# Kernel tuning notes

Measured on AMD Instinct MI355X. Metric: run time of the kernel, lower is better.

The kernel has to match this reference:

```python
import jax, jax.numpy as jnp
import numpy as np

K = 4
EPS = 1e-5
NEG_SLOPE = 0.2


def _edge_feature(coor_q, x_q, coor_k, x_k, k):
    """coor_*: [B,3,G*], x_q: [B,C,Gq], x_k: [B,C,Gk] -> [B,2C,Gq,k]"""
    B = x_k.shape[0]
    cq = jax.lax.stop_gradient(coor_q)
    ck = jax.lax.stop_gradient(coor_k)
    # squared pairwise distances [B, Gq, Gk]
    q2 = jnp.sum(cq * cq, axis=1)  # [B,Gq]
    k2 = jnp.sum(ck * ck, axis=1)  # [B,Gk]
    dist = q2[:, :, None] + k2[:, None, :] - 2.0 * jnp.einsum('bcq,bck->bqk', cq, ck)
    _, idx = jax.lax.top_k(-dist, k)  # k nearest, idx: [B,Gq,k]
    xk_t = jnp.transpose(x_k, (0, 2, 1))  # [B,Gk,C]
    feat = xk_t[jnp.arange(B)[:, None, None], idx]  # [B,Gq,k,C] gather
    feat = jnp.transpose(feat, (0, 3, 1, 2))  # [B,C,Gq,k]
    xq = jnp.broadcast_to(x_q[:, :, :, None], feat.shape)
    return jnp.concatenate([feat - xq, xq], axis=1)


def _group_norm(x, gamma, beta, groups):
    # x: [B,C,G,k], normalize per (group, sample) over (C//groups, G, k)
    B, C, G, k = x.shape
    xr = x.reshape(B, groups, -1)
    mean = jnp.mean(xr, axis=-1, keepdims=True)
    var = jnp.var(xr, axis=-1, keepdims=True)
    xn = ((xr - mean) * jax.lax.rsqrt(var + EPS)).reshape(B, C, G, k)
    return xn * gamma[None, :, None, None] + beta[None, :, None, None]


def _block(x, W, gamma, beta):
    # 1x1 conv (no bias) + GroupNorm(4) + LeakyReLU(0.2)
    y = jnp.einsum('oc,bcgk->bogk', W, x)
    y = _group_norm(y, gamma, beta, 4)
    return jax.nn.leaky_relu(y, NEG_SLOPE)


def setup_inputs() -> dict:
    key = jax.random.key(0)
    ks = jax.random.split(key, 10)
    B, C, Gs, Gd = 16, 384, 4096, 1024
    return {
        'coor': jax.random.normal(ks[0], (B, 3, Gs), jnp.float32),
        'f': jax.random.normal(ks[1], (B, C, Gs), jnp.float32),
        'coor_q': jax.random.normal(ks[2], (B, 3, Gd), jnp.float32),
        'f_q': jax.random.normal(ks[3], (B, C, Gd), jnp.float32),
        'W1': jax.random.normal(ks[4], (512, 2 * C), jnp.float32) * 0.02,
        'g1': jnp.ones((512,), jnp.float32),
        'b1': jnp.zeros((512,), jnp.float32),
        'W2': jax.random.normal(ks[5], (C, 1024), jnp.float32) * 0.02,
        'g2': jnp.ones((C,), jnp.float32),
        'b2': jnp.zeros((C,), jnp.float32),
    }


def reference(coor, f, coor_q, f_q, W1, g1, b1, W2, g2, b2):
    e1 = _edge_feature(coor_q, f_q, coor, f, K)        # [B,768,Gd,k]
    h = jnp.max(_block(e1, W1, g1, b1), axis=-1)       # [B,512,Gd]
    e2 = _edge_feature(coor_q, h, coor_q, h, K)        # [B,1024,Gd,k]
    out = jnp.max(_block(e2, W2, g2, b2), axis=-1)     # [B,384,Gd]
    return out
```

## Files before the change

kernel.cpp:

```cpp
#include <hip/hip_runtime.h>
#include <stdint.h>

#define B_   16
#define CIN  384
#define GS   4096
#define GD   1024
#define M1   512
#define K2C  512
#define M2   384
#define ROWS2 768
#define NEG  0.2f
#define EPS_ 1e-5f

typedef __bf16 bf16x8 __attribute__((ext_vector_type(8)));
typedef float  f32x4  __attribute__((ext_vector_type(4)));
typedef float  f32x2  __attribute__((ext_vector_type(2)));
typedef unsigned long long u64k;

__device__ __forceinline__ float bf2f(ushort u) {
  uint32_t v = ((uint32_t)u) << 16;
  return __builtin_bit_cast(float, v);
}
__device__ __forceinline__ ushort f2bf(float f) {
  uint32_t x = __builtin_bit_cast(uint32_t, f);
  x += 0x7FFFu + ((x >> 16) & 1u);
  return (ushort)(x >> 16);
}

__device__ __forceinline__ f32x2 pk_mul(f32x2 a, f32x2 b) {
  f32x2 d; asm("v_pk_mul_f32 %0, %1, %2" : "=v"(d) : "v"(a), "v"(b)); return d;
}
__device__ __forceinline__ f32x2 pk_add(f32x2 a, f32x2 b) {
  f32x2 d; asm("v_pk_add_f32 %0, %1, %2" : "=v"(d) : "v"(a), "v"(b)); return d;
}
__device__ __forceinline__ f32x2 pk_fma(f32x2 a, f32x2 b, f32x2 c) {
  f32x2 d; asm("v_pk_fma_f32 %0, %1, %2, %3" : "=v"(d) : "v"(a), "v"(b), "v"(c)); return d;
}

__device__ __forceinline__ void gload16(const void* g, void* l) {
  __builtin_amdgcn_global_load_lds(
      (const __attribute__((address_space(1))) void*)g,
      (__attribute__((address_space(3))) void*)l, 16, 0, 0);
}

__global__ void k_transpose(const float* __restrict__ src, ushort* __restrict__ dst,
                            int Cdim, int N) {
  __shared__ ushort tile[32][33];
  int b = blockIdx.z;
  int n0 = blockIdx.x * 32, c0 = blockIdx.y * 32;
  const float* s = src + (size_t)b * Cdim * N;
  ushort* d = dst + (size_t)b * Cdim * N;
  int tx = threadIdx.x, ty = threadIdx.y;
#pragma unroll
  for (int i = 0; i < 4; i++) {
    int c = c0 + ty + i * 8;
    tile[ty + i * 8][tx] = f2bf(s[(size_t)c * N + n0 + tx]);
  }
  __syncthreads();
#pragma unroll
  for (int i = 0; i < 4; i++) {
    int n = n0 + ty + i * 8;
    d[(size_t)n * Cdim + c0 + tx] = tile[tx][ty + i * 8];
  }
}

__global__ void k_wprep2(const float* __restrict__ W1, const float* __restrict__ W2,
                         ushort* __restrict__ W1a, ushort* __restrict__ W1d,
                         ushort* __restrict__ W2a, ushort* __restrict__ W2d) {
  int blk = blockIdx.x;
  if (blk < 768) {
    int t = blk * 256 + threadIdx.x;
    int o = t / 384, c = t % 384;
    float wa = W1[(size_t)o * 768 + c];
    float wb = W1[(size_t)o * 768 + 384 + c];
    W1a[t] = f2bf(wa);
    W1d[t] = f2bf(wb - wa);
  } else {
    int t = (blk - 768) * 256 + threadIdx.x;
    int o = t / 512, c = t % 512;
    float wa = W2[(size_t)o * 1024 + c];
    float wb = W2[(size_t)o * 1024 + 512 + c];
    W2a[t] = f2bf(wa);
    W2d[t] = f2bf(wb - wa);
  }
}

__global__ void k_s2both(const float* __restrict__ cs, const float* __restrict__ cq,
                         float* __restrict__ s2s, float* __restrict__ s2q) {
#pragma clang fp contract(off)
  int b = blockIdx.z;
  int i = blockIdx.x * 256 + threadIdx.x;
  if (i < GS) {
    const float* cb = cs + (size_t)b * 3 * GS;
    float x = cb[i], y = cb[GS + i], z = cb[2 * GS + i];
    s2s[(size_t)b * GS + i] = (x * x + y * y) + z * z;
  } else {
    int j = i - GS;
    const float* cb = cq + (size_t)b * 3 * GD;
    float x = cb[j], y = cb[GD + j], z = cb[2 * GD + j];
    s2q[(size_t)b * GD + j] = (x * x + y * y) + z * z;
  }
}

__device__ __forceinline__ uint32_t dmap(float d) {
  uint32_t u = __builtin_bit_cast(uint32_t, d);
  return u ^ (((uint32_t)((int32_t)u >> 31)) | 0x80000000u);
}
__device__ __forceinline__ u64k mkkey(uint32_t hi, uint32_t lo) {
  uint2 t; t.x = lo; t.y = hi;
  return __builtin_bit_cast(u64k, t);
}
__device__ __forceinline__ void kce(u64k& a, u64k& b) {
  bool c = b < a;
  u64k lo = c ? b : a, hi = c ? a : b;
  a = lo; b = hi;
}
__device__ __forceinline__ void klmin(u64k& a, u64k b) { a = b < a ? b : a; }

template<int GSRC>
__global__ __launch_bounds__(256) void k_knn(const float* __restrict__ cq,
                                             const float* __restrict__ ck,
                                             const float* __restrict__ s2qry,
                                             const float* __restrict__ s2src,
                                             int* __restrict__ idx) {
  constexpr int ITERS = GSRC / 256;
  static_assert(ITERS % 2 == 0, "even iteration count required for 2-deep unroll");
  int tid = threadIdx.x;
  int lane = tid & 63, wv = tid >> 6;
  int b = blockIdx.y;
  int qA = blockIdx.x * 8 + wv * 2;
  int qB = qA + 1;
  const float* cqb = cq + (size_t)b * 3 * GD;
  const float* ckb = ck + (size_t)b * 3 * GSRC;
  const float* s2b = s2src + (size_t)b * GSRC;
  float qxA = cqb[qA], qyA = cqb[GD + qA], qzA = cqb[2 * GD + qA];
  float qxB = cqb[qB], qyB = cqb[GD + qB], qzB = cqb[2 * GD + qB];
  float q2A = s2qry[(size_t)b * GD + qA];
  float q2B = s2qry[(size_t)b * GD + qB];
  f32x2 qxpA = {qxA, qxA}, qypA = {qyA, qyA}, qzpA = {qzA, qzA}, q2pA = {q2A, q2A};
  f32x2 qxpB = {qxB, qxB}, qypB = {qyB, qyB}, qzpB = {qzB, qzB}, q2pB = {q2B, q2B};
  f32x2 m2p = {-2.f, -2.f};

  u64k kA0 = ~0ull, kA1 = ~0ull, kA2 = ~0ull, kA3 = ~0ull;
  u64k kB0 = ~0ull, kB1 = ~0ull, kB2 = ~0ull, kB3 = ~0ull;

#define KNN_Q(QXP, QYP, QZP, Q2P, K0, K1, K2, K3)                              \
  {                                                                            \
    f32x2 dotl = pk_add(pk_add(pk_mul(QXP, xl), pk_mul(QYP, yl)), pk_mul(QZP, zl)); \
    f32x2 doth = pk_add(pk_add(pk_mul(QXP, xh), pk_mul(QYP, yh)), pk_mul(QZP, zh)); \
    f32x2 dl = pk_fma(dotl, m2p, pk_add(Q2P, sl));                             \
    f32x2 dh = pk_fma(doth, m2p, pk_add(Q2P, sh));                             \
    u64k n0 = mkkey(dmap(dl.x), j0u);                                          \
    u64k n1 = mkkey(dmap(dl.y), j0u + 1);                                      \
    u64k n2 = mkkey(dmap(dh.x), j0u + 2);                                      \
    u64k n3 = mkkey(dmap(dh.y), j0u + 3);                                      \
    kce(n0, n1); kce(n2, n3); kce(n0, n2); kce(n1, n3); kce(n1, n2);           \
    klmin(K0, n3); klmin(K1, n2); klmin(K2, n1); klmin(K3, n0);                \
    kce(K0, K2); kce(K1, K3); kce(K0, K1); kce(K2, K3);                        \
  }

#define KNN_STEP(Xv, Yv, Zv, Sv, J0)                                           \
  {                                                                            \
    f32x2 xl = {Xv.x, Xv.y}, xh = {Xv.z, Xv.w};                                \
    f32x2 yl = {Yv.x, Yv.y}, yh = {Yv.z, Yv.w};                                \
    f32x2 zl = {Zv.x, Zv.y}, zh = {Zv.z, Zv.w};                                \
    f32x2 sl = {Sv.x, Sv.y}, sh = {Sv.z, Sv.w};                                \
    uint32_t j0u = (uint32_t)(J0);                                             \
    KNN_Q(qxpA, qypA, qzpA, q2pA, kA0, kA1, kA2, kA3);                         \
    KNN_Q(qxpB, qypB, qzpB, q2pB, kB0, kB1, kB2, kB3);                         \
  }

#define KNN_LOAD(Xv, Yv, Zv, Sv, J)                                            \
  {                                                                            \
    Xv = *reinterpret_cast<const float4*>(ckb + (J));                          \
    Yv = *reinterpret_cast<const float4*>(ckb + GSRC + (J));                   \
    Zv = *reinterpret_cast<const float4*>(ckb + 2 * GSRC + (J));               \
    Sv = *reinterpret_cast<const float4*>(s2b + (J));                          \
  }

  int base = lane * 4;
  float4 X0, Y0, Z0, S0, X1, Y1, Z1, S1;
  KNN_LOAD(X0, Y0, Z0, S0, base);
  for (int it = 0; it < ITERS; it += 2) {
    int j0 = it * 256 + base;
    KNN_LOAD(X1, Y1, Z1, S1, j0 + 256);
    KNN_STEP(X0, Y0, Z0, S0, j0);
    if (it + 2 < ITERS) KNN_LOAD(X0, Y0, Z0, S0, j0 + 512);
    KNN_STEP(X1, Y1, Z1, S1, j0 + 256);
  }
#undef KNN_STEP
#undef KNN_Q
#undef KNN_LOAD

#pragma unroll
  for (int off = 1; off < 64; off <<= 1) {
    u64k p0 = __shfl_xor(kA0, off), p1 = __shfl_xor(kA1, off);
    u64k p2 = __shfl_xor(kA2, off), p3 = __shfl_xor(kA3, off);
    klmin(kA0, p3); klmin(kA1, p2); klmin(kA2, p1); klmin(kA3, p0);
    kce(kA0, kA2); kce(kA1, kA3); kce(kA0, kA1); kce(kA2, kA3);
    u64k r0 = __shfl_xor(kB0, off), r1 = __shfl_xor(kB1, off);
    u64k r2 = __shfl_xor(kB2, off), r3 = __shfl_xor(kB3, off);
    klmin(kB0, r3); klmin(kB1, r2); klmin(kB2, r1); klmin(kB3, r0);
    kce(kB0, kB2); kce(kB1, kB3); kce(kB0, kB1); kce(kB2, kB3);
  }
  if (lane == 0) {
    int4 ra;
    ra.x = (int)(uint32_t)kA0; ra.y = (int)(uint32_t)kA1;
    ra.z = (int)(uint32_t)kA2; ra.w = (int)(uint32_t)kA3;
    *reinterpret_cast<int4*>(&idx[((size_t)b * GD + qA) * 4]) = ra;
    int4 rb;
    rb.x = (int)(uint32_t)kB0; rb.y = (int)(uint32_t)kB1;
    rb.z = (int)(uint32_t)kB2; rb.w = (int)(uint32_t)kB3;
    *reinterpret_cast<int4*>(&idx[((size_t)b * GD + qB) * 4]) = rb;
  }
}

template<bool OUT_BF16>
__global__ __launch_bounds__(256) void k_gemm(const ushort* __restrict__ W,
                                              const ushort* __restrict__ Xt,
                                              void* __restrict__ outv,
                                              int M, int Kd, int N) {
  __shared__ __align__(16) ushort As[128 * 32];
  __shared__ __align__(16) ushort Bs[128 * 32];
  int b = blockIdx.z;
  const ushort* X = Xt + (size_t)b * N * Kd;
  int m0 = blockIdx.y * 128, n0 = blockIdx.x * 128;
  int tid = threadIdx.x;
  int w = tid >> 6, lane = tid & 63;
  int lr = lane & 15, lq = lane >> 4;
  int mw = (w >> 1) * 64, nw = (w & 1) * 64;
  int r0 = tid >> 2, c0 = tid & 3;

  ushort* dA0 = As + w * 512;
  ushort* dA1 = As + 2048 + w * 512;
  ushort* dB0 = Bs + w * 512;
  ushort* dB1 = Bs + 2048 + w * 512;
  const ushort* gA0 = W + (size_t)(m0 + r0) * Kd + c0 * 8;
  const ushort* gA1 = W + (size_t)(m0 + r0 + 64) * Kd + c0 * 8;
  const ushort* gB0 = X + (size_t)(n0 + r0) * Kd + c0 * 8;
  const ushort* gB1 = X + (size_t)(n0 + r0 + 64) * Kd + c0 * 8;

  f32x4 zero = {0.f, 0.f, 0.f, 0.f};
  f32x4 acc[4][4];
#pragma unroll
  for (int mi = 0; mi < 4; mi++)
#pragma unroll
    for (int ni = 0; ni < 4; ni++) acc[mi][ni] = zero;

  int nk = Kd / 32;
  for (int kt = 0; kt < nk; kt++) {
    int kk = kt * 32;
    __syncthreads();
    gload16(gA0 + kk, dA0);
    gload16(gA1 + kk, dA1);
    gload16(gB0 + kk, dB0);
    gload16(gB1 + kk, dB1);
    __syncthreads();
    bf16x8 af[4], bfr[4];
#pragma unroll
    for (int mi = 0; mi < 4; mi++)
      af[mi] = *reinterpret_cast<const bf16x8*>(&As[(mw + mi * 16 + lr) * 32 + lq * 8]);
#pragma unroll
    for (int ni = 0; ni < 4; ni++)
      bfr[ni] = *reinterpret_cast<const bf16x8*>(&Bs[(nw + ni * 16 + lr) * 32 + lq * 8]);
#pragma unroll
    for (int mi = 0; mi < 4; mi++)
#pragma unroll
      for (int ni = 0; ni < 4; ni++)
        acc[mi][ni] = __builtin_amdgcn_mfma_f32_16x16x32_bf16(af[mi], bfr[ni], acc[mi][ni], 0, 0, 0);
  }
#pragma unroll
  for (int mi = 0; mi < 4; mi++) {
    int m = m0 + mw + mi * 16 + lq * 4;
#pragma unroll
    for (int ni = 0; ni < 4; ni++) {
      int n = n0 + nw + ni * 16 + lr;
#pragma unroll
      for (int r = 0; r < 4; r++) {
        size_t off = (size_t)b * M * N + (size_t)(m + r) * N + n;
        if constexpr (OUT_BF16) ((ushort*)outv)[off] = f2bf(acc[mi][ni][r]);
        else                    ((float*)outv)[off] = acc[mi][ni][r];
      }
    }
  }
}

__global__ __launch_bounds__(256) void k_stats1y(const ushort* __restrict__ A,
                                                 const float* __restrict__ Bq,
                                                 const int* __restrict__ idx1,
                                                 const float* __restrict__ gam,
                                                 float* __restrict__ Ysel,
                                                 float* __restrict__ part) {
  __shared__ __align__(16) ushort Arow[GS];
  __shared__ __align__(16) int ids[GD * 4];
  __shared__ float rs[256], rq[256];
  int s = blockIdx.x, grp = blockIdx.y, b = blockIdx.z;
  int tid = threadIdx.x;
  for (int i = tid; i < GD; i += 256) {
    int4 v = *reinterpret_cast<const int4*>(&idx1[((size_t)b * GD + i) * 4]);
    v.x &= (GS - 1); v.y &= (GS - 1); v.z &= (GS - 1); v.w &= (GS - 1);
    *reinterpret_cast<int4*>(&ids[i * 4]) = v;
  }
  float sum = 0.f, ssq = 0.f;
  for (int oi = 0; oi < 16; oi++) {
    int o = grp * 128 + s * 16 + oi;
    const ushort* Ar = A + ((size_t)b * M1 + o) * GS;
    __syncthreads();
#pragma unroll
    for (int i = tid * 8; i < GS; i += 2048)
      *reinterpret_cast<uint4*>(&Arow[i]) = *reinterpret_cast<const uint4*>(&Ar[i]);
    __syncthreads();
    const float* Br = Bq + ((size_t)b * M1 + o) * GD;
    float* Yr = Ysel + ((size_t)b * M1 + o) * GD;
    float sgn = gam[o];
    for (int g = tid; g < GD; g += 256) {
      int4 id = *reinterpret_cast<const int4*>(&ids[g * 4]);
      float base = Br[g];
      float y0 = bf2f(Arow[id.x]) + base;
      float y1 = bf2f(Arow[id.y]) + base;
      float y2 = bf2f(Arow[id.z]) + base;
      float y3 = bf2f(Arow[id.w]) + base;
      sum += y0 + y1 + y2 + y3;
      ssq += y0 * y0 + y1 * y1 + y2 * y2 + y3 * y3;
      float mx = fmaxf(fmaxf(y0, y1), fmaxf(y2, y3));
      float mn = fminf(fminf(y0, y1), fminf(y2, y3));
      Yr[g] = (sgn >= 0.f) ? mx : mn;
    }
  }
  rs[tid] = sum; rq[tid] = ssq;
  __syncthreads();
  for (int t = 128; t > 0; t >>= 1) {
    if (tid < t) { rs[tid] += rs[tid + t]; rq[tid] += rq[tid + t]; }
    __syncthreads();
  }
  if (tid == 0) {
    int key = ((b * 4 + grp) * 8 + s) * 2;
    part[key] = rs[0]; part[key + 1] = rq[0];
  }
}

__global__ __launch_bounds__(256) void k_stats2y(const float* __restrict__ Y2,
                                                 const int* __restrict__ idx2,
                                                 const float* __restrict__ gam,
                                                 float* __restrict__ Ysel,
                                                 float* __restrict__ part) {
  __shared__ __align__(16) float Arow[GD];
  __shared__ __align__(16) int ids[GD * 4];
  __shared__ float rs[256], rq[256];
  int s = blockIdx.x, grp = blockIdx.y, b = blockIdx.z;
  int tid = threadIdx.x;
  for (int i = tid; i < GD; i += 256) {
    int4 v = *reinterpret_cast<const int4*>(&idx2[((size_t)b * GD + i) * 4]);
    v.x &= (GD - 1); v.y &= (GD - 1); v.z &= (GD - 1); v.w &= (GD - 1);
    *reinterpret_cast<int4*>(&ids[i * 4]) = v;
  }
  float sum = 0.f, ssq = 0.f;
  for (int oi = 0; oi < 12; oi++) {
    int o = grp * 96 + s * 12 + oi;
    const float* Ar = Y2 + ((size_t)b * ROWS2 + o) * GD;
    __syncthreads();
#pragma unroll
    for (int i = tid * 4; i < GD; i += 1024)
      *reinterpret_cast<float4*>(&Arow[i]) = *reinterpret_cast<const float4*>(&Ar[i]);
    __syncthreads();
    const float* Br = Y2 + ((size_t)b * ROWS2 + 384 + o) * GD;
    float* Yr = Ysel + ((size_t)b * M2 + o) * GD;
    float sgn = gam[o];
    for (int g = tid; g < GD; g += 256) {
      int4 id = *reinterpret_cast<const int4*>(&ids[g * 4]);
      float base = Br[g];
      float y0 = Arow[id.x] + base;
      float y1 = Arow[id.y] + base;
      float y2 = Arow[id.z] + base;
      float y3 = Arow[id.w] + base;
      sum += y0 + y1 + y2 + y3;
      ssq += y0 * y0 + y1 * y1 + y2 * y2 + y3 * y3;
      float mx = fmaxf(fmaxf(y0, y1), fmaxf(y2, y3));
      float mn = fminf(fminf(y0, y1), fminf(y2, y3));
      Yr[g] = (sgn >= 0.f) ? mx : mn;
    }
  }
  rs[tid] = sum; rq[tid] = ssq;
  __syncthreads();
  for (int t = 128; t > 0; t >>= 1) {
    if (tid < t) { rs[tid] += rs[tid + t]; rq[tid] += rq[tid + t]; }
    __syncthreads();
  }
  if (tid == 0) {
    int key = ((b * 4 + grp) * 8 + s) * 2;
    part[key] = rs[0]; part[key + 1] = rq[0];
  }
}

__global__ void k_h2(const float* __restrict__ Ysel, const float* __restrict__ part,
                     const float* __restrict__ gam, const float* __restrict__ bet,
                     ushort* __restrict__ hT) {
  __shared__ ushort tile[64][66];
  int g0 = blockIdx.x * 64, o0 = blockIdx.y * 64, b = blockIdx.z;
  int tid = threadIdx.x;
  int tkey = b * 4 + (o0 >> 7);
  float s = 0.f, q = 0.f;
#pragma unroll
  for (int i = 0; i < 8; i++) { s += part[(tkey * 8 + i) * 2]; q += part[(tkey * 8 + i) * 2 + 1]; }
  float mean = s * (1.0f / 524288.0f);
  float var = q * (1.0f / 524288.0f) - mean * mean;
  float rstd = 1.0f / sqrtf(fmaxf(var, 0.0f) + EPS_);
  int gx = tid & 63, oy = tid >> 6;
#pragma unroll
  for (int oi = 0; oi < 16; oi++) {
    int ol = oi * 4 + oy;
    int o = o0 + ol;
    float y = Ysel[((size_t)b * M1 + o) * GD + g0 + gx];
    float v = (y - mean) * rstd * gam[o] + bet[o];
    v = v >= 0.f ? v : NEG * v;
    tile[ol][gx] = f2bf(v);
  }
  __syncthreads();
  int col = tid & 63, r4 = tid >> 6;
#pragma unroll
  for (int i = 0; i < 16; i++) {
    int gl = i * 4 + r4;
    hT[((size_t)b * GD + g0 + gl) * K2C + o0 + col] = tile[col][gl];
  }
}

__global__ void k_out2(const float* __restrict__ Ysel2, const float* __restrict__ part,
                       const float* __restrict__ gam, const float* __restrict__ bet,
                       float* __restrict__ out) {
  int b = blockIdx.z, o = blockIdx.y;
  int g = blockIdx.x * 256 + threadIdx.x;
  int tkey = b * 4 + o / 96;
  float s = 0.f, q = 0.f;
#pragma unroll
  for (int i = 0; i < 8; i++) { s += part[(tkey * 8 + i) * 2]; q += part[(tkey * 8 + i) * 2 + 1]; }
  float mean = s * (1.0f / 393216.0f);
  float var = q * (1.0f / 393216.0f) - mean * mean;
  float rstd = 1.0f / sqrtf(fmaxf(var, 0.0f) + EPS_);
  float y = Ysel2[((size_t)b * M2 + o) * GD + g];
  float v = (y - mean) * rstd * gam[o] + bet[o];
  v = v >= 0.f ? v : NEG * v;
  out[((size_t)b * M2 + o) * GD + g] = v;
}

extern "C" void kernel_launch(void* const* d_in, const int* in_sizes, int n_in,
                              void* d_out, int out_size, void* d_ws, size_t ws_size,
                              hipStream_t stream) {
  (void)in_sizes; (void)n_in; (void)out_size;
  const float* coor  = (const float*)d_in[0];
  const float* f     = (const float*)d_in[1];
  const float* coorq = (const float*)d_in[2];
  const float* fq    = (const float*)d_in[3];
  const float* W1    = (const float*)d_in[4];
  const float* g1    = (const float*)d_in[5];
  const float* b1    = (const float*)d_in[6];
  const float* W2    = (const float*)d_in[7];
  const float* g2    = (const float*)d_in[8];
  const float* b2    = (const float*)d_in[9];

  if (ws_size < 182468608u) return;

  char* ws = (char*)d_ws;
  int*    idx1 = (int*)(ws + 0);
  int*    idx2 = (int*)(ws + 0x40000);
  float*  s1p  = (float*)(ws + 0x80000);
  float*  s2p  = (float*)(ws + 0x82000);
  ushort* W1a  = (ushort*)(ws + 0x84000);
  ushort* W1d  = W1a + (size_t)512 * 384;
  ushort* W2a  = W1d + (size_t)512 * 384;
  ushort* W2d  = W2a + (size_t)384 * 512;
  ushort* fT   = W2d + (size_t)384 * 512;
  ushort* fqT  = fT + (size_t)B_ * GS * CIN;
  ushort* Abuf = fqT + (size_t)B_ * GD * CIN;
  float*  Bq   = (float*)(Abuf + (size_t)B_ * M1 * GS);
  ushort* hT   = (ushort*)((char*)Bq + (size_t)B_ * M1 * GD * 4);
  float*  Y2   = (float*)fT;
  float*  Ysel1 = (float*)fT;
  float*  Ysel2 = (float*)Abuf;
  float*  s2s  = (float*)hT;
  float*  s2q  = s2s + (size_t)B_ * GS;

  k_transpose<<<dim3(GS / 32, CIN / 32, B_), dim3(32, 8), 0, stream>>>(f, fT, CIN, GS);
  k_transpose<<<dim3(GD / 32, CIN / 32, B_), dim3(32, 8), 0, stream>>>(fq, fqT, CIN, GD);
  k_wprep2<<<dim3(1536), 256, 0, stream>>>(W1, W2, W1a, W1d, W2a, W2d);
  k_s2both<<<dim3((GS + GD) / 256, 1, B_), 256, 0, stream>>>(coor, coorq, s2s, s2q);

  k_knn<GS><<<dim3(GD / 8, B_), 256, 0, stream>>>(coorq, coor, s2q, s2s, idx1);
  k_knn<GD><<<dim3(GD / 8, B_), 256, 0, stream>>>(coorq, coorq, s2q, s2q, idx2);

  k_gemm<true ><<<dim3(GS / 128, M1 / 128, B_), 256, 0, stream>>>(W1a, fT, Abuf, M1, CIN, GS);
  k_gemm<false><<<dim3(GD / 128, M1 / 128, B_), 256, 0, stream>>>(W1d, fqT, Bq, M1, CIN, GD);

  k_stats1y<<<dim3(8, 4, B_), 256, 0, stream>>>(Abuf, Bq, idx1, g1, Ysel1, s1p);
  k_h2<<<dim3(GD / 64, M1 / 64, B_), 256, 0, stream>>>(Ysel1, s1p, g1, b1, hT);

  k_gemm<false><<<dim3(GD / 128, ROWS2 / 128, B_), 256, 0, stream>>>(W2a, hT, Y2, ROWS2, K2C, GD);

  k_stats2y<<<dim3(8, 4, B_), 256, 0, stream>>>(Y2, idx2, g2, Ysel2, s2p);
  k_out2<<<dim3(GD / 256, M2, B_), 256, 0, stream>>>(Ysel2, s2p, g2, b2, (float*)d_out);
}
```

Baseline: 452.5 us.

## Fuse input transpose into first GEMM and merge prep kernels

Removes the two standalone transpose kernels that converted f and f_q to bf16 [N,C] layout. A new GEMM variant reads fp32 inputs in their [C,N] layout directly, converts them to bf16 and packs them into padded shared memory. It also merges the weight prep and squared-norm kernels into one launch. This saves a full read/write pass over the large feature tensors and several launches. In exchange, the B-operand load in the GEMM becomes a scalar, non-async fp32 load with conversion inside the main loop, which may slow the GEMM itself.

```diff
diff --git a/kernel.cpp b/kernel.cpp
--- a/kernel.cpp
+++ b/kernel.cpp
@@ -43,30 +43,12 @@
       (__attribute__((address_space(3))) void*)l, 16, 0, 0);
 }
 
-__global__ void k_transpose(const float* __restrict__ src, ushort* __restrict__ dst,
-                            int Cdim, int N) {
-  __shared__ ushort tile[32][33];
-  int b = blockIdx.z;
-  int n0 = blockIdx.x * 32, c0 = blockIdx.y * 32;
-  const float* s = src + (size_t)b * Cdim * N;
-  ushort* d = dst + (size_t)b * Cdim * N;
-  int tx = threadIdx.x, ty = threadIdx.y;
-#pragma unroll
-  for (int i = 0; i < 4; i++) {
-    int c = c0 + ty + i * 8;
-    tile[ty + i * 8][tx] = f2bf(s[(size_t)c * N + n0 + tx]);
-  }
-  __syncthreads();
-#pragma unroll
-  for (int i = 0; i < 4; i++) {
-    int n = n0 + ty + i * 8;
-    d[(size_t)n * Cdim + c0 + tx] = tile[tx][ty + i * 8];
-  }
-}
-
-__global__ void k_wprep2(const float* __restrict__ W1, const float* __restrict__ W2,
-                         ushort* __restrict__ W1a, ushort* __restrict__ W1d,
-                         ushort* __restrict__ W2a, ushort* __restrict__ W2d) {
+__global__ void k_prep(const float* __restrict__ W1, const float* __restrict__ W2,
+                       ushort* __restrict__ W1a, ushort* __restrict__ W1d,
+                       ushort* __restrict__ W2a, ushort* __restrict__ W2d,
+                       const float* __restrict__ cs, const float* __restrict__ cqv,
+                       float* __restrict__ s2s, float* __restrict__ s2q) {
+#pragma clang fp contract(off)
   int blk = blockIdx.x;
   if (blk < 768) {
     int t = blk * 256 + threadIdx.x;
@@ -75,30 +57,27 @@
     float wb = W1[(size_t)o * 768 + 384 + c];
     W1a[t] = f2bf(wa);
     W1d[t] = f2bf(wb - wa);
-  } else {
+  } else if (blk < 1536) {
     int t = (blk - 768) * 256 + threadIdx.x;
     int o = t / 512, c = t % 512;
     float wa = W2[(size_t)o * 1024 + c];
     float wb = W2[(size_t)o * 1024 + 512 + c];
     W2a[t] = f2bf(wa);
     W2d[t] = f2bf(wb - wa);
-  }
-}
-
-__global__ void k_s2both(const float* __restrict__ cs, const float* __restrict__ cq,
-                         float* __restrict__ s2s, float* __restrict__ s2q) {
-#pragma clang fp contract(off)
-  int b = blockIdx.z;
-  int i = blockIdx.x * 256 + threadIdx.x;
-  if (i < GS) {
-    const float* cb = cs + (size_t)b * 3 * GS;
-    float x = cb[i], y = cb[GS + i], z = cb[2 * GS + i];
-    s2s[(size_t)b * GS + i] = (x * x + y * y) + z * z;
   } else {
-    int j = i - GS;
-    const float* cb = cq + (size_t)b * 3 * GD;
-    float x = cb[j], y = cb[GD + j], z = cb[2 * GD + j];
-    s2q[(size_t)b * GD + j] = (x * x + y * y) + z * z;
+    int u = blk - 1536;
+    int b = u / 20;
+    int i = (u % 20) * 256 + threadIdx.x;
+    if (i < GS) {
+      const float* cb = cs + (size_t)b * 3 * GS;
+      float x = cb[i], y = cb[GS + i], z = cb[2 * GS + i];
+      s2s[(size_t)b * GS + i] = (x * x + y * y) + z * z;
+    } else {
+      int j = i - GS;
+      const float* cb = cqv + (size_t)b * 3 * GD;
+      float x = cb[j], y = cb[GD + j], z = cb[2 * GD + j];
+      s2q[(size_t)b * GD + j] = (x * x + y * y) + z * z;
+    }
   }
 }
 
@@ -216,6 +195,82 @@
 }
 
 template<bool OUT_BF16>
+__global__ __launch_bounds__(256) void k_gemmF(const ushort* __restrict__ W,
+                                               const float* __restrict__ X32,
+                                               void* __restrict__ outv,
+                                               int M, int Kd, int N) {
+  __shared__ __align__(16) ushort As[128 * 32];
+  __shared__ __align__(16) ushort Bs[128 * 40];
+  int b = blockIdx.z;
+  const float* X = X32 + (size_t)b * Kd * N;
+  int m0 = blockIdx.y * 128, n0 = blockIdx.x * 128;
+  int tid = threadIdx.x;
+  int w = tid >> 6, lane = tid & 63;
+  int lr = lane & 15, lq = lane >> 4;
+  int mw = (w >> 1) * 64, nw = (w & 1) * 64;
+  int r0 = tid >> 2, c0 = tid & 3;
+
+  ushort* dA0 = As + w * 512;
+  ushort* dA1 = As + 2048 + w * 512;
+  const ushort* gA0 = W + (size_t)(m0 + r0) * Kd + c0 * 8;
+  const ushort* gA1 = W + (size_t)(m0 + r0 + 64) * Kd + c0 * 8;
+
+  int bn = tid & 127;
+  int bm = tid >> 7;
+
+  f32x4 zero = {0.f, 0.f, 0.f, 0.f};
+  f32x4 acc[4][4];
+#pragma unroll
+  for (int mi = 0; mi < 4; mi++)
+#pragma unroll
+    for (int ni = 0; ni < 4; ni++) acc[mi][ni] = zero;
+
+  int nk = Kd / 32;
+  for (int kt = 0; kt < nk; kt++) {
+    int kk = kt * 32;
+    __syncthreads();
+    gload16(gA0 + kk, dA0);
+    gload16(gA1 + kk, dA1);
+#pragma unroll
+    for (int pp = 0; pp < 8; pp++) {
+      int m = pp * 2 + bm;
+      int k = kk + 2 * m;
+      float va = X[(size_t)k * N + n0 + bn];
+      float vb = X[(size_t)(k + 1) * N + n0 + bn];
+      ushort2 pkv; pkv.x = f2bf(va); pkv.y = f2bf(vb);
+      *reinterpret_cast<ushort2*>(&Bs[bn * 40 + 2 * m]) = pkv;
+    }
+    __syncthreads();
+    bf16x8 af[4], bfr[4];
+#pragma unroll
+    for (int mi = 0; mi < 4; mi++)
+      af[mi] = *reinterpret_cast<const bf16x8*>(&As[(mw + mi * 16 + lr) * 32 + lq * 8]);
+#pragma unroll
+    for (int ni = 0; ni < 4; ni++)
+      bfr[ni] = *reinterpret_cast<const bf16x8*>(&Bs[(nw + ni * 16 + lr) * 40 + lq * 8]);
+#pragma unroll
+    for (int mi = 0; mi < 4; mi++)
+#pragma unroll
+      for (int ni = 0; ni < 4; ni++)
+        acc[mi][ni] = __builtin_amdgcn_mfma_f32_16x16x32_bf16(af[mi], bfr[ni], acc[mi][ni], 0, 0, 0);
+  }
+#pragma unroll
+  for (int mi = 0; mi < 4; mi++) {
+    int m = m0 + mw + mi * 16 + lq * 4;
+#pragma unroll
+    for (int ni = 0; ni < 4; ni++) {
+      int n = n0 + nw + ni * 16 + lr;
+#pragma unroll
+      for (int r = 0; r < 4; r++) {
+        size_t off = (size_t)b * M * N + (size_t)(m + r) * N + n;
+        if constexpr (OUT_BF16) ((ushort*)outv)[off] = f2bf(acc[mi][ni][r]);
+        else                    ((float*)outv)[off] = acc[mi][ni][r];
+      }
+    }
+  }
+}
+
+template<bool OUT_BF16>
 __global__ __launch_bounds__(256) void k_gemm(const ushort* __restrict__ W,
                                               const ushort* __restrict__ Xt,
                                               void* __restrict__ outv,
@@ -479,16 +534,14 @@
   float*  s2s  = (float*)hT;
   float*  s2q  = s2s + (size_t)B_ * GS;
 
-  k_transpose<<<dim3(GS / 32, CIN / 32, B_), dim3(32, 8), 0, stream>>>(f, fT, CIN, GS);
-  k_transpose<<<dim3(GD / 32, CIN / 32, B_), dim3(32, 8), 0, stream>>>(fq, fqT, CIN, GD);
-  k_wprep2<<<dim3(1536), 256, 0, stream>>>(W1, W2, W1a, W1d, W2a, W2d);
-  k_s2both<<<dim3((GS + GD) / 256, 1, B_), 256, 0, stream>>>(coor, coorq, s2s, s2q);
+  k_prep<<<dim3(1856), 256, 0, stream>>>(W1, W2, W1a, W1d, W2a, W2d,
+                                         coor, coorq, s2s, s2q);
 
   k_knn<GS><<<dim3(GD / 8, B_), 256, 0, stream>>>(coorq, coor, s2q, s2s, idx1);
   k_knn<GD><<<dim3(GD / 8, B_), 256, 0, stream>>>(coorq, coorq, s2q, s2q, idx2);
 
-  k_gemm<true ><<<dim3(GS / 128, M1 / 128, B_), 256, 0, stream>>>(W1a, fT, Abuf, M1, CIN, GS);
-  k_gemm<false><<<dim3(GD / 128, M1 / 128, B_), 256, 0, stream>>>(W1d, fqT, Bq, M1, CIN, GD);
+  k_gemmF<true ><<<dim3(GS / 128, M1 / 128, B_), 256, 0, stream>>>(W1a, f, Abuf, M1, CIN, GS);
+  k_gemmF<false><<<dim3(GD / 128, M1 / 128, B_), 256, 0, stream>>>(W1d, fq, Bq, M1, CIN, GD);
 
   k_stats1y<<<dim3(8, 4, B_), 256, 0, stream>>>(Abuf, Bq, idx1, g1, Ysel1, s1p);
   k_h2<<<dim3(GD / 64, M1 / 64, B_), 256, 0, stream>>>(Ysel1, s1p, g1, b1, hT);
```

Result: faster. 438.1 us (-3.2%).
